# Performance work log

Measured on AMD Instinct MI355X. Metric: run time of the kernel, lower is better.

The kernel has to match this reference:

```python
import jax, jax.numpy as jnp
import numpy as np

N_NODES = 100000
N_EDGES = 2000000
D = 128
HIDDEN = 128


def setup_inputs() -> dict:
    key = jax.random.key(0)
    k_src, k_dst, k_idx, k_w1, k_w2 = jax.random.split(key, 5)
    src = jax.random.normal(k_src, (N_NODES, D), dtype=jnp.float32)
    dst = jax.random.normal(k_dst, (N_NODES, D), dtype=jnp.float32)
    edge_label_index = jax.random.randint(k_idx, (2, N_EDGES), 0, N_NODES, dtype=jnp.int64)
    # Kaiming-ish init for the two linear layers
    W1 = jax.random.normal(k_w1, (D, HIDDEN), dtype=jnp.float32) / np.sqrt(D)
    b1 = jnp.zeros((HIDDEN,), dtype=jnp.float32)
    W2 = jax.random.normal(k_w2, (HIDDEN, 1), dtype=jnp.float32) / np.sqrt(HIDDEN)
    b2 = jnp.zeros((1,), dtype=jnp.float32)
    return {"src": src, "dst": dst, "edge_label_index": edge_label_index,
            "W1": W1, "b1": b1, "W2": W2, "b2": b2}


def reference(src, dst, edge_label_index, W1, b1, W2, b2):
    row = edge_label_index[0]
    col = edge_label_index[1]
    # gather endpoint embeddings and fuse with elementwise product: [E, D]
    z = src[row] * dst[col]
    # 2-layer MLP; dropout p=0 is the identity
    h = jax.nn.relu(z @ W1 + b1)           # [E, HIDDEN]
    out = h @ W2 + b2                       # [E, 1]
    return out.reshape(-1)                  # [E]
```

## Files before the change

kernel.cpp:

```cpp
#include <hip/hip_runtime.h>
#include <hip/hip_bf16.h>
#include <hip/hip_fp16.h>

typedef __attribute__((ext_vector_type(8))) _Float16 half8;
typedef __attribute__((ext_vector_type(4))) float f32x4;

#define BLOCK 256
#define GTILE 16
#define NBKT  32

__device__ __forceinline__ int swz16(int row, int boff) {
    return (row << 8) + (boff ^ ((row & 15) << 4));
}
__device__ __forceinline__ int swzH(int row, int boff) {
    return (row << 7) + (boff ^ ((row & 7) << 4));
}

__device__ __forceinline__ int probe_i64(const int* eli) {
    int any = 0;
    #pragma unroll
    for (int i = 0; i < 32; ++i) any |= eli[2 * i + 1];
    return (any == 0) ? 1 : 0;
}

__global__ __launch_bounds__(256) void cvt_hist_kernel(
    const float* __restrict__ a, const float* __restrict__ b,
    _Float16* __restrict__ oa, _Float16* __restrict__ ob, int n,
    const int* __restrict__ eli, int E, float scale, unsigned int* __restrict__ cnt)
{
    __shared__ unsigned int h[NBKT];
    __shared__ int s_i64;
    if (threadIdx.x < NBKT) h[threadIdx.x] = 0;
    if (threadIdx.x == 0) s_i64 = probe_i64(eli);
    __syncthreads();

    const int i = blockIdx.x * blockDim.x + threadIdx.x;
    const int stride = gridDim.x * blockDim.x;
    const float4* a4 = (const float4*)a;
    const float4* b4 = (const float4*)b;
    const int n8 = n >> 3;
    for (int j = i; j < n8; j += stride) {
        float4 x0 = a4[2 * j], x1 = a4[2 * j + 1];
        float4 y0 = b4[2 * j], y1 = b4[2 * j + 1];
        union { _Float16 hh[8]; uint4 u; } pa, pb;
        pa.hh[0]=(_Float16)x0.x; pa.hh[1]=(_Float16)x0.y;
        pa.hh[2]=(_Float16)x0.z; pa.hh[3]=(_Float16)x0.w;
        pa.hh[4]=(_Float16)x1.x; pa.hh[5]=(_Float16)x1.y;
        pa.hh[6]=(_Float16)x1.z; pa.hh[7]=(_Float16)x1.w;
        pb.hh[0]=(_Float16)y0.x; pb.hh[1]=(_Float16)y0.y;
        pb.hh[2]=(_Float16)y0.z; pb.hh[3]=(_Float16)y0.w;
        pb.hh[4]=(_Float16)y1.x; pb.hh[5]=(_Float16)y1.y;
        pb.hh[6]=(_Float16)y1.z; pb.hh[7]=(_Float16)y1.w;
        ((uint4*)oa)[j] = pa.u;
        ((uint4*)ob)[j] = pb.u;
    }
    for (int j = (n8 << 3) + i; j < n; j += stride) {
        oa[j] = (_Float16)a[j];
        ob[j] = (_Float16)b[j];
    }
    const int i64f = s_i64;
    for (int e = i; e < E; e += stride) {
        int c = i64f ? eli[2 * ((size_t)E + e)] : eli[(size_t)E + e];
        int bkt = (int)((float)c * scale);
        if (bkt > NBKT - 1) bkt = NBKT - 1;
        atomicAdd(&h[bkt], 1u);
    }
    __syncthreads();
    if (threadIdx.x < NBKT && h[threadIdx.x])
        atomicAdd(&cnt[threadIdx.x], h[threadIdx.x]);
}

__global__ void scan_kernel(const unsigned int* __restrict__ cnt,
                            unsigned int* __restrict__ segStart,
                            unsigned int* __restrict__ cursor)
{
    if (threadIdx.x == 0) {
        unsigned int s = 0;
        for (int b = 0; b < NBKT; ++b) { segStart[b] = s; cursor[b] = s; s += cnt[b]; }
        segStart[NBKT] = s;
    }
}

__global__ __launch_bounds__(256) void scatter_kernel(
    const int* __restrict__ eli, int E, float scale,
    unsigned int* __restrict__ cursor,
    uint2* __restrict__ sorted, unsigned int* __restrict__ inv)
{
    __shared__ unsigned int lcnt[NBKT];
    __shared__ unsigned int lpos[NBKT];
    __shared__ int s_i64;
    if (threadIdx.x < NBKT) lcnt[threadIdx.x] = 0;
    if (threadIdx.x == 0) s_i64 = probe_i64(eli);
    __syncthreads();
    const int i64f = s_i64;

    const int chunk = (E + gridDim.x - 1) / gridDim.x;
    const int e0 = blockIdx.x * chunk;
    const int e1 = min(E, e0 + chunk);

    for (int e = e0 + threadIdx.x; e < e1; e += blockDim.x) {
        int c = i64f ? eli[2 * ((size_t)E + e)] : eli[(size_t)E + e];
        int bkt = (int)((float)c * scale);
        if (bkt > NBKT - 1) bkt = NBKT - 1;
        atomicAdd(&lcnt[bkt], 1u);
    }
    __syncthreads();
    if (threadIdx.x < NBKT) {
        unsigned int nv = lcnt[threadIdx.x];
        lpos[threadIdx.x] = nv ? atomicAdd(&cursor[threadIdx.x], nv) : 0u;
    }
    __syncthreads();
    for (int e = e0 + threadIdx.x; e < e1; e += blockDim.x) {
        int r, c;
        if (i64f) { r = eli[2 * (size_t)e]; c = eli[2 * ((size_t)E + e)]; }
        else      { r = eli[e];             c = eli[(size_t)E + e]; }
        int bkt = (int)((float)c * scale);
        if (bkt > NBKT - 1) bkt = NBKT - 1;
        unsigned int pos = atomicAdd(&lpos[bkt], 1u);
        sorted[pos] = make_uint2((unsigned)r, (unsigned)c);
        inv[e] = pos;
    }
}

__global__ __launch_bounds__(BLOCK, 3) void mlp_sorted_kernel(
    const _Float16* __restrict__ srcb, const _Float16* __restrict__ dstb,
    const uint2* __restrict__ sorted, const unsigned int* __restrict__ segStart,
    const float* __restrict__ W1, const float* __restrict__ b1,
    const float* __restrict__ W2, const float* __restrict__ b2,
    float* __restrict__ tmp, int E)
{
    __shared__ __align__(16) char lds[49152];

    const int tid  = threadIdx.x;
    const int lane = tid & 63;
    const int w    = tid >> 6;
    const int rr   = lane & 15;
    const int kgrp = lane >> 4;
    const int rq8  = lane >> 3;
    const int cl   = lane & 7;

    for (int idx = tid; idx < 128 * 128; idx += BLOCK) {
        int k = idx >> 7, n = idx & 127;
        *(_Float16*)(lds + swz16(n, k * 2)) = (_Float16)W1[idx];
    }
    __syncthreads();

    char* zb = lds + 32768 + (w << 12);

    float b1s[8], w2s[8];
    #pragma unroll
    for (int cb = 0; cb < 8; ++cb) {
        b1s[cb] = b1[cb * 16 + rr];
        w2s[cb] = W2[cb * 16 + rr];
    }
    const float bias2 = b2[0];

    const int x     = blockIdx.x & 7;
    const int kb    = blockIdx.x >> 3;
    const int nbs   = gridDim.x >> 3;
    const int wslot = kb * 4 + w;
    const int wstep = nbs * 4;

    half8 sv[4], dv[4];
    const half8* s8 = (const half8*)srcb;
    const half8* d8 = (const half8*)dstb;

    for (int j = 0; j < NBKT / 8; ++j) {
        const int b  = x + 8 * j;
        const int s0 = (int)segStart[b];
        const int s1 = (int)segStart[b + 1];
        if (s1 <= s0) continue;
        const int nt = (s1 - s0 + 15) >> 4;
        int t = wslot;
        if (t >= nt) continue;

        {
            int idx = s0 + t * 16 + rr; if (idx >= s1) idx = s1 - 1;
            uint2 iv = sorted[idx];
            #pragma unroll
            for (int i = 0; i < 4; ++i) {
                int hr = i * 8 + rq8, e = hr >> 1, hh = hr & 1;
                int r = __shfl((int)iv.x, e, 64);
                int c = __shfl((int)iv.y, e, 64);
                sv[i] = s8[(size_t)r * 16 + hh * 8 + cl];
                dv[i] = d8[(size_t)c * 16 + hh * 8 + cl];
            }
        }

        while (true) {
            const int base = s0 + t * 16;
            int cnt = s1 - base; if (cnt > 16) cnt = 16;

            asm volatile("" ::: "memory");
            #pragma unroll
            for (int i = 0; i < 4; ++i) {
                int hr = i * 8 + rq8;
                half8 pr = sv[i] * dv[i];
                *(half8*)(zb + swzH(hr, cl * 16)) = pr;
            }

            const int tn = t + wstep;
            if (tn < nt) {
                int idx = s0 + tn * 16 + rr; if (idx >= s1) idx = s1 - 1;
                uint2 iv = sorted[idx];
                #pragma unroll
                for (int i = 0; i < 4; ++i) {
                    int hr = i * 8 + rq8, e = hr >> 1, hh = hr & 1;
                    int r = __shfl((int)iv.x, e, 64);
                    int c = __shfl((int)iv.y, e, 64);
                    sv[i] = s8[(size_t)r * 16 + hh * 8 + cl];
                    dv[i] = d8[(size_t)c * 16 + hh * 8 + cl];
                }
            }
            asm volatile("" ::: "memory");

            f32x4 acc[8];
            #pragma unroll
            for (int cb = 0; cb < 8; ++cb) acc[cb] = (f32x4){0.f, 0.f, 0.f, 0.f};
            __builtin_amdgcn_s_setprio(1);
            #pragma unroll
            for (int kk = 0; kk < 4; ++kk) {
                half8 af = *(const half8*)(zb + swzH(rr * 2 + (kk >> 1),
                                                     (kk & 1) * 64 + kgrp * 16));
                #pragma unroll
                for (int cb = 0; cb < 8; ++cb) {
                    half8 bf = *(const half8*)(lds + swz16(cb * 16 + rr,
                                                           kk * 64 + kgrp * 16));
                    acc[cb] = __builtin_amdgcn_mfma_f32_16x16x32_f16(af, bf, acc[cb], 0, 0, 0);
                }
            }
            __builtin_amdgcn_s_setprio(0);

            #pragma unroll
            for (int r = 0; r < 4; ++r) {
                float p = 0.f;
                #pragma unroll
                for (int cb = 0; cb < 8; ++cb) {
                    float hv = acc[cb][r] + b1s[cb];
                    hv = fmaxf(hv, 0.f);
                    p = fmaf(hv, w2s[cb], p);
                }
                p += __shfl_xor(p, 1, 64);
                p += __shfl_xor(p, 2, 64);
                p += __shfl_xor(p, 4, 64);
                p += __shfl_xor(p, 8, 64);
                int eo = kgrp * 4 + r;
                if (rr == 0 && eo < cnt)
                    __builtin_nontemporal_store(p + bias2, &tmp[base + eo]);
            }
            if (tn >= nt) break;
            t = tn;
        }
    }
}

__global__ __launch_bounds__(256) void permute_kernel(
    const float* __restrict__ tmp, const unsigned int* __restrict__ inv,
    float* __restrict__ out, int E)
{
    for (int e = blockIdx.x * blockDim.x + threadIdx.x; e < E;
         e += gridDim.x * blockDim.x)
        out[e] = tmp[inv[e]];
}

template<int MODE>
__global__ __launch_bounds__(BLOCK, 3) void edge_mlp_fb(
    const float* __restrict__ srcf, const float* __restrict__ dstf,
    const _Float16* __restrict__ srcb, const _Float16* __restrict__ dstb,
    const int* __restrict__ eli,
    const float* __restrict__ W1, const float* __restrict__ b1,
    const float* __restrict__ W2, const float* __restrict__ b2,
    float* __restrict__ out, int E)
{
    __shared__ __align__(16) char lds[49152];
    const int tid  = threadIdx.x;
    const int lane = tid & 63;
    const int w    = tid >> 6;
    const int rr   = lane & 15;
    const int kgrp = lane >> 4;
    const int rq8  = lane >> 3;
    const int cl   = lane & 7;

    for (int idx = tid; idx < 128 * 128; idx += BLOCK) {
        int k = idx >> 7, n = idx & 127;
        *(_Float16*)(lds + swz16(n, k * 2)) = (_Float16)W1[idx];
    }
    int probe = eli[2 * (lane & 31) + 1];
    unsigned long long bl = __ballot(lane < 32 && probe != 0);
    const int i64f = (bl == 0ull) ? 1 : 0;
    __syncthreads();

    char* zb = lds + 32768 + (w << 12);
    float b1s[8], w2s[8];
    #pragma unroll
    for (int cb = 0; cb < 8; ++cb) {
        b1s[cb] = b1[cb * 16 + rr];
        w2s[cb] = W2[cb * 16 + rr];
    }
    const float bias2 = b2[0];

    const int ngroups = (E + GTILE - 1) / GTILE;
    const int step = gridDim.x * 4;
    int g = blockIdx.x * 4 + w;
    if (g >= ngroups) return;

    auto idxload = [&](int gg) -> int {
        gg = gg < ngroups ? gg : ngroups - 1;
        int e = gg * GTILE + rr; if (e >= E) e = E - 1;
        size_t off = (lane < 32) ? (size_t)e : (size_t)E + (size_t)e;
        return i64f ? eli[2 * off] : eli[off];
    };

    half8 sv[4], dv[4];
    auto loadT = [&](int iv) {
        const half8* s8 = (const half8*)srcb;
        const half8* d8 = (const half8*)dstb;
        #pragma unroll
        for (int i = 0; i < 4; ++i) {
            int hr = i * 8 + rq8, e = hr >> 1, hh = hr & 1;
            int r = __shfl(iv, e, 64);
            int c = __shfl(iv, 32 + e, 64);
            sv[i] = s8[(size_t)r * 16 + hh * 8 + cl];
            dv[i] = d8[(size_t)c * 16 + hh * 8 + cl];
        }
    };
    auto stageF = [&](int iv) {
        const float4* s4 = (const float4*)srcf;
        const float4* d4 = (const float4*)dstf;
        #pragma unroll
        for (int i = 0; i < 4; ++i) {
            int hr = i * 8 + rq8, e = hr >> 1, hh = hr & 1;
            int r = __shfl(iv, e, 64);
            int c = __shfl(iv, 32 + e, 64);
            float4 a0 = s4[(size_t)r * 32 + hh * 16 + cl * 2];
            float4 a1 = s4[(size_t)r * 32 + hh * 16 + cl * 2 + 1];
            float4 c0 = d4[(size_t)c * 32 + hh * 16 + cl * 2];
            float4 c1 = d4[(size_t)c * 32 + hh * 16 + cl * 2 + 1];
            union { _Float16 hf[8]; half8 v; } pr;
            pr.hf[0]=(_Float16)(a0.x*c0.x); pr.hf[1]=(_Float16)(a0.y*c0.y);
            pr.hf[2]=(_Float16)(a0.z*c0.z); pr.hf[3]=(_Float16)(a0.w*c0.w);
            pr.hf[4]=(_Float16)(a1.x*c1.x); pr.hf[5]=(_Float16)(a1.y*c1.y);
            pr.hf[6]=(_Float16)(a1.z*c1.z); pr.hf[7]=(_Float16)(a1.w*c1.w);
            *(half8*)(zb + swzH(hr, cl * 16)) = pr.v;
        }
    };
    auto compute = [&](int gg) {
        f32x4 acc[8];
        #pragma unroll
        for (int cb = 0; cb < 8; ++cb) acc[cb] = (f32x4){0.f, 0.f, 0.f, 0.f};
        __builtin_amdgcn_s_setprio(1);
        #pragma unroll
        for (int kk = 0; kk < 4; ++kk) {
            half8 af = *(const half8*)(zb + swzH(rr * 2 + (kk >> 1),
                                                 (kk & 1) * 64 + kgrp * 16));
            #pragma unroll
            for (int cb = 0; cb < 8; ++cb) {
                half8 bf = *(const half8*)(lds + swz16(cb * 16 + rr,
                                                       kk * 64 + kgrp * 16));
                acc[cb] = __builtin_amdgcn_mfma_f32_16x16x32_f16(af, bf, acc[cb], 0, 0, 0);
            }
        }
        __builtin_amdgcn_s_setprio(0);
        #pragma unroll
        for (int r = 0; r < 4; ++r) {
            float p = 0.f;
            #pragma unroll
            for (int cb = 0; cb < 8; ++cb) {
                float hv = acc[cb][r] + b1s[cb];
                hv = fmaxf(hv, 0.f);
                p = fmaf(hv, w2s[cb], p);
            }
            p += __shfl_xor(p, 1, 64);
            p += __shfl_xor(p, 2, 64);
            p += __shfl_xor(p, 4, 64);
            p += __shfl_xor(p, 8, 64);
            int e = gg * GTILE + kgrp * 4 + r;
            if (rr == 0 && e < E)
                __builtin_nontemporal_store(p + bias2, &out[e]);
        }
    };

    if constexpr (MODE == 1) {
        int iv = idxload(g);
        loadT(iv);
        while (true) {
            asm volatile("" ::: "memory");
            #pragma unroll
            for (int i = 0; i < 4; ++i) {
                int hr = i * 8 + rq8;
                half8 pr = sv[i] * dv[i];
                *(half8*)(zb + swzH(hr, cl * 16)) = pr;
            }
            int gn = g + step;
            if (gn < ngroups) { int iv2 = idxload(gn); loadT(iv2); }
            asm volatile("" ::: "memory");
            compute(g);
            if (gn >= ngroups) break;
            g = gn;
        }
    } else {
        for (; g < ngroups; g += step) {
            asm volatile("" ::: "memory");
            int iv = idxload(g);
            stageF(iv);
            asm volatile("" ::: "memory");
            compute(g);
        }
    }
}

extern "C" void kernel_launch(void* const* d_in, const int* in_sizes, int n_in,
                              void* d_out, int out_size, void* d_ws, size_t ws_size,
                              hipStream_t stream) {
    const float* src = (const float*)d_in[0];
    const float* dst = (const float*)d_in[1];
    const int*   eli = (const int*)d_in[2];
    const float* W1  = (const float*)d_in[3];
    const float* b1  = (const float*)d_in[4];
    const float* W2  = (const float*)d_in[5];
    const float* b2  = (const float*)d_in[6];
    float* out = (float*)d_out;

    const int E = in_sizes[2] / 2;
    const int n = in_sizes[0];
    const int N = n / 128;
    const float scale = (float)NBKT / (float)N;

    const size_t NB = (size_t)n * sizeof(_Float16);
    const size_t need_full = 4096 + 2 * NB + (size_t)E * 16;
    const size_t need_tab  = 2 * NB;

    if (ws_size >= need_full) {
        char* wsb = (char*)d_ws;
        unsigned int* cnt      = (unsigned int*)wsb;
        unsigned int* segStart = cnt + 32;
        unsigned int* cursor   = segStart + 40;
        _Float16* srcb = (_Float16*)(wsb + 4096);
        _Float16* dstb = srcb + n;
        uint2* sorted  = (uint2*)(wsb + 4096 + 2 * NB);
        unsigned int* inv = (unsigned int*)(sorted + E);
        float* tmp = (float*)(inv + E);

        hipMemsetAsync(wsb, 0, 4096, stream);
        cvt_hist_kernel<<<dim3(2048), dim3(256), 0, stream>>>(
            src, dst, srcb, dstb, n, eli, E, scale, cnt);
        scan_kernel<<<dim3(1), dim3(64), 0, stream>>>(cnt, segStart, cursor);
        scatter_kernel<<<dim3(256), dim3(256), 0, stream>>>(
            eli, E, scale, cursor, sorted, inv);
        mlp_sorted_kernel<<<dim3(768), dim3(BLOCK), 0, stream>>>(
            srcb, dstb, sorted, segStart, W1, b1, W2, b2, tmp, E);
        permute_kernel<<<dim3(2048), dim3(256), 0, stream>>>(tmp, inv, out, E);
    } else if (ws_size >= need_tab) {
        _Float16* srcb = (_Float16*)d_ws;
        _Float16* dstb = srcb + n;
        if (ws_size >= need_tab + 4096) {
            char* wsb = (char*)d_ws;
            unsigned int* cnt = (unsigned int*)(wsb + 2 * NB);
            _Float16* sb = (_Float16*)wsb;
            _Float16* db = sb + n;
            hipMemsetAsync(cnt, 0, 4096, stream);
            cvt_hist_kernel<<<dim3(2048), dim3(256), 0, stream>>>(
                src, dst, sb, db, n, eli, E, scale, cnt);
            const int ngroups = (E + GTILE - 1) / GTILE;
            int nblocks = (ngroups + 3) / 4;
            int grid = nblocks < 768 ? nblocks : 768;
            edge_mlp_fb<1><<<dim3(grid), dim3(BLOCK), 0, stream>>>(
                src, dst, sb, db, eli, W1, b1, W2, b2, out, E);
        } else {
            const int ngroups = (E + GTILE - 1) / GTILE;
            int nblocks = (ngroups + 3) / 4;
            int grid = nblocks < 768 ? nblocks : 768;
            edge_mlp_fb<0><<<dim3(grid), dim3(BLOCK), 0, stream>>>(
                src, dst, (const _Float16*)nullptr, (const _Float16*)nullptr,
                eli, W1, b1, W2, b2, out, E);
        }
    } else {
        const int ngroups = (E + GTILE - 1) / GTILE;
        int nblocks = (ngroups + 3) / 4;
        int grid = nblocks < 768 ? nblocks : 768;
        edge_mlp_fb<0><<<dim3(grid), dim3(BLOCK), 0, stream>>>(
            src, dst, (const _Float16*)nullptr, (const _Float16*)nullptr,
            eli, W1, b1, W2, b2, out, E);
    }
}
```

Before: 200.9 us.

## Pack edge ids into sorted records and scatter outputs directly, dropping permute pass

Each sorted record now packs row, col (17 bits each) and the original edge index into one uint2, so the MLP kernel writes results straight to their final output position. This removes the separate inv array, the tmp buffer and the permute kernel, saving a launch and several E-sized reads and writes. The MLP loop also gains double-buffered gathers that prefetch two tiles ahead. In exchange the output stores become scattered rather than contiguous, the path only applies when N and E fit the bit packing, and register pressure rises from the extra buffers.

```diff
diff --git a/kernel.cpp b/kernel.cpp
--- a/kernel.cpp
+++ b/kernel.cpp
@@ -83,8 +83,7 @@
 
 __global__ __launch_bounds__(256) void scatter_kernel(
     const int* __restrict__ eli, int E, float scale,
-    unsigned int* __restrict__ cursor,
-    uint2* __restrict__ sorted, unsigned int* __restrict__ inv)
+    unsigned int* __restrict__ cursor, uint2* __restrict__ sorted)
 {
     __shared__ unsigned int lcnt[NBKT];
     __shared__ unsigned int lpos[NBKT];
@@ -117,8 +116,9 @@
         int bkt = (int)((float)c * scale);
         if (bkt > NBKT - 1) bkt = NBKT - 1;
         unsigned int pos = atomicAdd(&lpos[bkt], 1u);
-        sorted[pos] = make_uint2((unsigned)r, (unsigned)c);
-        inv[e] = pos;
+        unsigned lo = (unsigned)r | ((unsigned)c << 17);
+        unsigned hi = ((unsigned)c >> 15) | ((unsigned)e << 2);
+        sorted[pos] = make_uint2(lo, hi);
     }
 }
 
@@ -127,7 +127,7 @@
     const uint2* __restrict__ sorted, const unsigned int* __restrict__ segStart,
     const float* __restrict__ W1, const float* __restrict__ b1,
     const float* __restrict__ W2, const float* __restrict__ b2,
-    float* __restrict__ tmp, int E)
+    float* __restrict__ out, int E)
 {
     __shared__ __align__(16) char lds[49152];
 
@@ -161,106 +161,106 @@
     const int wslot = kb * 4 + w;
     const int wstep = nbs * 4;
 
-    half8 sv[4], dv[4];
     const half8* s8 = (const half8*)srcb;
     const half8* d8 = (const half8*)dstb;
 
+    half8 svA[4], dvA[4], svB[4], dvB[4];
+    int eoA = 0, eoB = 0;
+    int s0 = 0, s1 = 0;
+
+    auto loadT = [&](int t, half8 (&s)[4], half8 (&d)[4], int& eo) {
+        int idx = s0 + t * 16 + rr; if (idx >= s1) idx = s1 - 1;
+        uint2 pk = sorted[idx];
+        int r = (int)(pk.x & 0x1FFFFu);
+        int c = (int)(((pk.x >> 17) | (pk.y << 15)) & 0x1FFFFu);
+        eo = (int)(pk.y >> 2);
+        #pragma unroll
+        for (int i = 0; i < 4; ++i) {
+            int hr = i * 8 + rq8, e = hr >> 1, hh = hr & 1;
+            int rn = __shfl(r, e, 64);
+            int cn = __shfl(c, e, 64);
+            s[i] = s8[(size_t)rn * 16 + hh * 8 + cl];
+            d[i] = d8[(size_t)cn * 16 + hh * 8 + cl];
+        }
+    };
+    auto writeZ = [&](const half8 (&s)[4], const half8 (&d)[4]) {
+        #pragma unroll
+        for (int i = 0; i < 4; ++i) {
+            int hr = i * 8 + rq8;
+            half8 pr = s[i] * d[i];
+            *(half8*)(zb + swzH(hr, cl * 16)) = pr;
+        }
+    };
+    auto compute = [&](int base, int eoCur) {
+        int cnt = s1 - base; if (cnt > 16) cnt = 16;
+        f32x4 acc[8];
+        #pragma unroll
+        for (int cb = 0; cb < 8; ++cb) acc[cb] = (f32x4){0.f, 0.f, 0.f, 0.f};
+        __builtin_amdgcn_s_setprio(1);
+        #pragma unroll
+        for (int kk = 0; kk < 4; ++kk) {
+            half8 af = *(const half8*)(zb + swzH(rr * 2 + (kk >> 1),
+                                                 (kk & 1) * 64 + kgrp * 16));
+            #pragma unroll
+            for (int cb = 0; cb < 8; ++cb) {
+                half8 bf = *(const half8*)(lds + swz16(cb * 16 + rr,
+                                                       kk * 64 + kgrp * 16));
+                acc[cb] = __builtin_amdgcn_mfma_f32_16x16x32_f16(af, bf, acc[cb], 0, 0, 0);
+            }
+        }
+        __builtin_amdgcn_s_setprio(0);
+        #pragma unroll
+        for (int r = 0; r < 4; ++r) {
+            float p = 0.f;
+            #pragma unroll
+            for (int cb = 0; cb < 8; ++cb) {
+                float hv = acc[cb][r] + b1s[cb];
+                hv = fmaxf(hv, 0.f);
+                p = fmaf(hv, w2s[cb], p);
+            }
+            p += __shfl_xor(p, 1, 64);
+            p += __shfl_xor(p, 2, 64);
+            p += __shfl_xor(p, 4, 64);
+            p += __shfl_xor(p, 8, 64);
+            int es = kgrp * 4 + r;
+            int eOrig = __shfl(eoCur, es, 64);
+            if (rr == 0 && es < cnt)
+                out[eOrig] = p + bias2;
+        }
+    };
+
     for (int j = 0; j < NBKT / 8; ++j) {
-        const int b  = x + 8 * j;
-        const int s0 = (int)segStart[b];
-        const int s1 = (int)segStart[b + 1];
+        const int b = x + 8 * j;
+        s0 = (int)segStart[b];
+        s1 = (int)segStart[b + 1];
         if (s1 <= s0) continue;
         const int nt = (s1 - s0 + 15) >> 4;
         int t = wslot;
         if (t >= nt) continue;
 
-        {
-            int idx = s0 + t * 16 + rr; if (idx >= s1) idx = s1 - 1;
-            uint2 iv = sorted[idx];
-            #pragma unroll
-            for (int i = 0; i < 4; ++i) {
-                int hr = i * 8 + rq8, e = hr >> 1, hh = hr & 1;
-                int r = __shfl((int)iv.x, e, 64);
-                int c = __shfl((int)iv.y, e, 64);
-                sv[i] = s8[(size_t)r * 16 + hh * 8 + cl];
-                dv[i] = d8[(size_t)c * 16 + hh * 8 + cl];
-            }
-        }
+        loadT(t, svA, dvA, eoA);
+        if (t + wstep < nt) loadT(t + wstep, svB, dvB, eoB);
 
         while (true) {
-            const int base = s0 + t * 16;
-            int cnt = s1 - base; if (cnt > 16) cnt = 16;
-
-            asm volatile("" ::: "memory");
-            #pragma unroll
-            for (int i = 0; i < 4; ++i) {
-                int hr = i * 8 + rq8;
-                half8 pr = sv[i] * dv[i];
-                *(half8*)(zb + swzH(hr, cl * 16)) = pr;
-            }
-
-            const int tn = t + wstep;
-            if (tn < nt) {
-                int idx = s0 + tn * 16 + rr; if (idx >= s1) idx = s1 - 1;
-                uint2 iv = sorted[idx];
-                #pragma unroll
-                for (int i = 0; i < 4; ++i) {
-                    int hr = i * 8 + rq8, e = hr >> 1, hh = hr & 1;
-                    int r = __shfl((int)iv.x, e, 64);
-                    int c = __shfl((int)iv.y, e, 64);
-                    sv[i] = s8[(size_t)r * 16 + hh * 8 + cl];
-                    dv[i] = d8[(size_t)c * 16 + hh * 8 + cl];
-                }
-            }
-            asm volatile("" ::: "memory");
-
-            f32x4 acc[8];
-            #pragma unroll
-            for (int cb = 0; cb < 8; ++cb) acc[cb] = (f32x4){0.f, 0.f, 0.f, 0.f};
-            __builtin_amdgcn_s_setprio(1);
-            #pragma unroll
-            for (int kk = 0; kk < 4; ++kk) {
-                half8 af = *(const half8*)(zb + swzH(rr * 2 + (kk >> 1),
-                                                     (kk & 1) * 64 + kgrp * 16));
-                #pragma unroll
-                for (int cb = 0; cb < 8; ++cb) {
-                    half8 bf = *(const half8*)(lds + swz16(cb * 16 + rr,
-                                                           kk * 64 + kgrp * 16));
-                    acc[cb] = __builtin_amdgcn_mfma_f32_16x16x32_f16(af, bf, acc[cb], 0, 0, 0);
-                }
-            }
-            __builtin_amdgcn_s_setprio(0);
-
-            #pragma unroll
-            for (int r = 0; r < 4; ++r) {
-                float p = 0.f;
-                #pragma unroll
-                for (int cb = 0; cb < 8; ++cb) {
-                    float hv = acc[cb][r] + b1s[cb];
-                    hv = fmaxf(hv, 0.f);
-                    p = fmaf(hv, w2s[cb], p);
-                }
-                p += __shfl_xor(p, 1, 64);
-                p += __shfl_xor(p, 2, 64);
-                p += __shfl_xor(p, 4, 64);
-                p += __shfl_xor(p, 8, 64);
-                int eo = kgrp * 4 + r;
-                if (rr == 0 && eo < cnt)
-                    __builtin_nontemporal_store(p + bias2, &tmp[base + eo]);
-            }
-            if (tn >= nt) break;
-            t = tn;
-        }
-    }
-}
-
-__global__ __launch_bounds__(256) void permute_kernel(
-    const float* __restrict__ tmp, const unsigned int* __restrict__ inv,
-    float* __restrict__ out, int E)
-{
-    for (int e = blockIdx.x * blockDim.x + threadIdx.x; e < E;
-         e += gridDim.x * blockDim.x)
-        out[e] = tmp[inv[e]];
+            asm volatile("" ::: "memory");
+            writeZ(svA, dvA);
+            int eoCur = eoA;
+            int tp = t + 2 * wstep;
+            if (tp < nt) loadT(tp, svA, dvA, eoA);
+            asm volatile("" ::: "memory");
+            compute(s0 + t * 16, eoCur);
+            t += wstep; if (t >= nt) break;
+
+            asm volatile("" ::: "memory");
+            writeZ(svB, dvB);
+            eoCur = eoB;
+            tp = t + 2 * wstep;
+            if (tp < nt) loadT(tp, svB, dvB, eoB);
+            asm volatile("" ::: "memory");
+            compute(s0 + t * 16, eoCur);
+            t += wstep; if (t >= nt) break;
+        }
+    }
 }
 
 template<int MODE>
@@ -375,8 +375,7 @@
             p += __shfl_xor(p, 4, 64);
             p += __shfl_xor(p, 8, 64);
             int e = gg * GTILE + kgrp * 4 + r;
-            if (rr == 0 && e < E)
-                __builtin_nontemporal_store(p + bias2, &out[e]);
+            if (rr == 0 && e < E) out[e] = p + bias2;
         }
     };
 
@@ -427,10 +426,11 @@
     const float scale = (float)NBKT / (float)N;
 
     const size_t NB = (size_t)n * sizeof(_Float16);
-    const size_t need_full = 4096 + 2 * NB + (size_t)E * 16;
-    const size_t need_tab  = 2 * NB;
-
-    if (ws_size >= need_full) {
+    const size_t need_full = 4096 + 2 * NB + (size_t)E * 8;
+    const size_t need_tab  = 2 * NB + 4096;
+    const bool packable = (N <= 131072) && (E < (1 << 29));
+
+    if (ws_size >= need_full && packable) {
         char* wsb = (char*)d_ws;
         unsigned int* cnt      = (unsigned int*)wsb;
         unsigned int* segStart = cnt + 32;
@@ -438,42 +438,28 @@
         _Float16* srcb = (_Float16*)(wsb + 4096);
         _Float16* dstb = srcb + n;
         uint2* sorted  = (uint2*)(wsb + 4096 + 2 * NB);
-        unsigned int* inv = (unsigned int*)(sorted + E);
-        float* tmp = (float*)(inv + E);
 
         hipMemsetAsync(wsb, 0, 4096, stream);
         cvt_hist_kernel<<<dim3(2048), dim3(256), 0, stream>>>(
             src, dst, srcb, dstb, n, eli, E, scale, cnt);
         scan_kernel<<<dim3(1), dim3(64), 0, stream>>>(cnt, segStart, cursor);
         scatter_kernel<<<dim3(256), dim3(256), 0, stream>>>(
-            eli, E, scale, cursor, sorted, inv);
+            eli, E, scale, cursor, sorted);
         mlp_sorted_kernel<<<dim3(768), dim3(BLOCK), 0, stream>>>(
-            srcb, dstb, sorted, segStart, W1, b1, W2, b2, tmp, E);
-        permute_kernel<<<dim3(2048), dim3(256), 0, stream>>>(tmp, inv, out, E);
+            srcb, dstb, sorted, segStart, W1, b1, W2, b2, out, E);
     } else if (ws_size >= need_tab) {
-        _Float16* srcb = (_Float16*)d_ws;
-        _Float16* dstb = srcb + n;
-        if (ws_size >= need_tab + 4096) {
-            char* wsb = (char*)d_ws;
-            unsigned int* cnt = (unsigned int*)(wsb + 2 * NB);
-            _Float16* sb = (_Float16*)wsb;
-            _Float16* db = sb + n;
-            hipMemsetAsync(cnt, 0, 4096, stream);
-            cvt_hist_kernel<<<dim3(2048), dim3(256), 0, stream>>>(
-                src, dst, sb, db, n, eli, E, scale, cnt);
-            const int ngroups = (E + GTILE - 1) / GTILE;
-            int nblocks = (ngroups + 3) / 4;
-            int grid = nblocks < 768 ? nblocks : 768;
-            edge_mlp_fb<1><<<dim3(grid), dim3(BLOCK), 0, stream>>>(
-                src, dst, sb, db, eli, W1, b1, W2, b2, out, E);
-        } else {
-            const int ngroups = (E + GTILE - 1) / GTILE;
-            int nblocks = (ngroups + 3) / 4;
-            int grid = nblocks < 768 ? nblocks : 768;
-            edge_mlp_fb<0><<<dim3(grid), dim3(BLOCK), 0, stream>>>(
-                src, dst, (const _Float16*)nullptr, (const _Float16*)nullptr,
-                eli, W1, b1, W2, b2, out, E);
-        }
+        char* wsb = (char*)d_ws;
+        unsigned int* cnt = (unsigned int*)(wsb + 2 * NB);
+        _Float16* sb = (_Float16*)wsb;
+        _Float16* db = sb + n;
+        hipMemsetAsync(cnt, 0, 4096, stream);
+        cvt_hist_kernel<<<dim3(2048), dim3(256), 0, stream>>>(
+            src, dst, sb, db, n, eli, E, scale, cnt);
+        const int ngroups = (E + GTILE - 1) / GTILE;
+        int nblocks = (ngroups + 3) / 4;
+        int grid = nblocks < 768 ? nblocks : 768;
+        edge_mlp_fb<1><<<dim3(grid), dim3(BLOCK), 0, stream>>>(
+            src, dst, sb, db, eli, W1, b1, W2, b2, out, E);
     } else {
         const int ngroups = (E + GTILE - 1) / GTILE;
         int nblocks = (ngroups + 3) / 4;
```

Measured after the change: 206.0 us. 2.5% more time.
